# Kernel optimization log

Measured on AMD Instinct MI355X. Metric: run time of the kernel, lower is better.

## Reference

```python
import jax, jax.numpy as jnp
import numpy as np

B, T, D = 32, 512, 384
DUR_MAX = 8                 # durations drawn in [0, DUR_MAX)
MAX_OUT = T * (DUR_MAX - 1) # static upper bound on total expanded length (3584)
ALPHA = 1.0


def setup_inputs() -> dict:
    key = jax.random.key(0)
    k1, k2 = jax.random.split(key)
    x = jax.random.normal(k1, (B, T, D), dtype=jnp.float32)
    durations = jax.random.randint(k2, (B, T), 0, DUR_MAX, dtype=jnp.int32)
    return {"input": x, "durations": durations}


def reference(input, durations):
    # patched_dur = clamp(round(alpha * dur), min=0)
    patched = jnp.round(ALPHA * durations.astype(jnp.float32)).astype(jnp.int32)
    patched = jnp.maximum(patched, 0)                       # [B, T]
    cum = jnp.cumsum(patched, axis=1)                       # [B, T] exclusive-right boundaries
    total = cum[:, -1:]                                      # [B, 1] true expanded lengths

    pos = jnp.arange(MAX_OUT, dtype=jnp.int32)               # [MAX_OUT]
    # output frame j comes from token idx = first t with cum[t] > j
    idx = jax.vmap(lambda c: jnp.searchsorted(c, pos, side='right'))(cum)  # [B, MAX_OUT]
    idx = jnp.clip(idx, 0, T - 1)
    valid = pos[None, :] < total                              # [B, MAX_OUT]

    out = jnp.take_along_axis(input, idx[:, :, None], axis=1)  # [B, MAX_OUT, D]
    return jnp.where(valid[:, :, None], out, jnp.zeros((), dtype=input.dtype))
```

## Files before the change

### kernel.cpp

```cpp
#include <hip/hip_runtime.h>

typedef float v4f __attribute__((ext_vector_type(4)));

#define NB 32
#define NT 512
#define ND 384
#define MAX_OUT 3584
#define NV 96
#define TILE 64
#define BLK 256
#define PER (TILE * NV / BLK)
#define TILES_PER_B (MAX_OUT / TILE)

__global__ __launch_bounds__(NT) void lr_scan_scatter(
    const int* __restrict__ dur, int* __restrict__ totals, int* __restrict__ idxmap)
{
    __shared__ int wsum[NT / 64];
    const int b = blockIdx.x;
    const int t = threadIdx.x;
    const int lane = t & 63;
    const int w = t >> 6;

    int d = dur[b * NT + t];
    d = d > 0 ? d : 0;

    int c = d;
    #pragma unroll
    for (int off = 1; off < 64; off <<= 1) {
        int v = __shfl_up(c, off, 64);
        if (lane >= off) c += v;
    }
    if (lane == 63) wsum[w] = c;
    __syncthreads();

    int add = 0;
    for (int i = 0; i < w; ++i) add += wsum[i];
    const int cum = c + add;
    const int start = cum - d;

    int* base = idxmap + b * MAX_OUT;
    for (int j = 0; j < d; ++j) base[start + j] = t;

    if (t == NT - 1) totals[b] = cum;
}

__global__ __launch_bounds__(BLK) void lr_gather(
    const v4f* __restrict__ in, const int* __restrict__ totals,
    const int* __restrict__ idxmap, v4f* __restrict__ out)
{
    const unsigned g8 = gridDim.x >> 3;
    const unsigned blk = (blockIdx.x & 7u) * g8 + (blockIdx.x >> 3);

    const unsigned b    = blk / TILES_PER_B;
    const unsigned tile = blk - b * TILES_PER_B;
    const unsigned row0 = tile * TILE;

    __shared__ int sidx[TILE];
    __shared__ int stot;
    const int t = threadIdx.x;
    if (t < TILE) sidx[t] = idxmap[b * MAX_OUT + row0 + t];
    if (t == 0)   stot = totals[b];
    __syncthreads();

    const int nvalid = stot - (int)row0;
    const v4f* inb  = in  + (size_t)b * NT * NV;
    v4f*       outb = out + ((size_t)b * MAX_OUT + row0) * NV;

    if (nvalid >= TILE) {
        #pragma unroll
        for (int k = 0; k < PER; ++k) {
            const int i = t + k * BLK;
            const int r = i / NV;
            const int c = i - r * NV;
            const v4f v = inb[sidx[r] * NV + c];
            __builtin_nontemporal_store(v, outb + i);
        }
    } else if (nvalid <= 0) {
        const v4f z = {0.f, 0.f, 0.f, 0.f};
        #pragma unroll
        for (int k = 0; k < PER; ++k)
            __builtin_nontemporal_store(z, outb + t + k * BLK);
    } else {
        #pragma unroll
        for (int k = 0; k < PER; ++k) {
            const int i = t + k * BLK;
            const int r = i / NV;
            const int c = i - r * NV;
            v4f v = {0.f, 0.f, 0.f, 0.f};
            if (r < nvalid) v = inb[sidx[r] * NV + c];
            __builtin_nontemporal_store(v, outb + i);
        }
    }
}

extern "C" void kernel_launch(void* const* d_in, const int* in_sizes, int n_in,
                              void* d_out, int out_size, void* d_ws, size_t ws_size,
                              hipStream_t stream)
{
    const float* x   = (const float*)d_in[0];
    const int*   dur = (const int*)d_in[1];

    int* totals = (int*)d_ws;
    int* idxmap = (int*)((char*)d_ws + 128);

    lr_scan_scatter<<<NB, NT, 0, stream>>>(dur, totals, idxmap);

    const unsigned n_blk = (unsigned)NB * TILES_PER_B;
    lr_gather<<<n_blk, BLK, 0, stream>>>(
        (const v4f*)x, totals, idxmap, (v4f*)d_out);
}
```

Before: 207.7 us.

## Fuse duration scan into gather kernel with per-block binary search

```diff
diff --git a/kernel.cpp b/kernel.cpp
--- a/kernel.cpp
+++ b/kernel.cpp
@@ -12,57 +12,60 @@
 #define PER (TILE * NV / BLK)
 #define TILES_PER_B (MAX_OUT / TILE)
 
-__global__ __launch_bounds__(NT) void lr_scan_scatter(
-    const int* __restrict__ dur, int* __restrict__ totals, int* __restrict__ idxmap)
+__global__ __launch_bounds__(BLK) void lr_fused(
+    const int* __restrict__ dur, const v4f* __restrict__ in, v4f* __restrict__ out)
 {
-    __shared__ int wsum[NT / 64];
-    const int b = blockIdx.x;
-    const int t = threadIdx.x;
+    const unsigned g8  = gridDim.x >> 3;
+    const unsigned blk = (blockIdx.x & 7u) * g8 + (blockIdx.x >> 3);
+    const unsigned b    = blk / TILES_PER_B;
+    const unsigned tile = blk - b * TILES_PER_B;
+    const unsigned row0 = tile * TILE;
+
+    __shared__ int cum[NT];
+    __shared__ int wpart[BLK / 64];
+    __shared__ int sidx[TILE];
+
+    const int t    = threadIdx.x;
     const int lane = t & 63;
-    const int w = t >> 6;
+    const int w    = t >> 6;
 
-    int d = dur[b * NT + t];
-    d = d > 0 ? d : 0;
-
-    int c = d;
+    const int2 dd = ((const int2*)(dur + b * NT))[t];
+    const int d0 = dd.x > 0 ? dd.x : 0;
+    const int d1 = dd.y > 0 ? dd.y : 0;
+    const int s = d0 + d1;
+    int c = s;
     #pragma unroll
     for (int off = 1; off < 64; off <<= 1) {
         int v = __shfl_up(c, off, 64);
         if (lane >= off) c += v;
     }
-    if (lane == 63) wsum[w] = c;
+    if (lane == 63) wpart[w] = c;
+    __syncthreads();
+    int add = 0;
+    #pragma unroll
+    for (int i = 0; i < BLK / 64; ++i) if (i < w) add += wpart[i];
+    const int epfx = add + c - s;
+    cum[2 * t]     = epfx + d0;
+    cum[2 * t + 1] = epfx + d0 + d1;
     __syncthreads();
 
-    int add = 0;
-    for (int i = 0; i < w; ++i) add += wsum[i];
-    const int cum = c + add;
-    const int start = cum - d;
+    const int total = cum[NT - 1];
 
-    int* base = idxmap + b * MAX_OUT;
-    for (int j = 0; j < d; ++j) base[start + j] = t;
-
-    if (t == NT - 1) totals[b] = cum;
-}
-
-__global__ __launch_bounds__(BLK) void lr_gather(
-    const v4f* __restrict__ in, const int* __restrict__ totals,
-    const int* __restrict__ idxmap, v4f* __restrict__ out)
-{
-    const unsigned g8 = gridDim.x >> 3;
-    const unsigned blk = (blockIdx.x & 7u) * g8 + (blockIdx.x >> 3);
-
-    const unsigned b    = blk / TILES_PER_B;
-    const unsigned tile = blk - b * TILES_PER_B;
-    const unsigned row0 = tile * TILE;
-
-    __shared__ int sidx[TILE];
-    __shared__ int stot;
-    const int t = threadIdx.x;
-    if (t < TILE) sidx[t] = idxmap[b * MAX_OUT + row0 + t];
-    if (t == 0)   stot = totals[b];
+    if (t < TILE) {
+        const int pos = (int)row0 + t;
+        int lo = 0, hi = NT;
+        #pragma unroll
+        for (int step = 0; step < 10; ++step) {
+            if (lo < hi) {
+                const int mid = (lo + hi) >> 1;
+                if (cum[mid] <= pos) lo = mid + 1; else hi = mid;
+            }
+        }
+        sidx[t] = lo < NT - 1 ? lo : NT - 1;
+    }
     __syncthreads();
 
-    const int nvalid = stot - (int)row0;
+    const int nvalid = total - (int)row0;
     const v4f* inb  = in  + (size_t)b * NT * NV;
     v4f*       outb = out + ((size_t)b * MAX_OUT + row0) * NV;
 
@@ -71,8 +74,8 @@
         for (int k = 0; k < PER; ++k) {
             const int i = t + k * BLK;
             const int r = i / NV;
-            const int c = i - r * NV;
-            const v4f v = inb[sidx[r] * NV + c];
+            const int c2 = i - r * NV;
+            const v4f v = inb[sidx[r] * NV + c2];
             __builtin_nontemporal_store(v, outb + i);
         }
     } else if (nvalid <= 0) {
@@ -85,9 +88,9 @@
         for (int k = 0; k < PER; ++k) {
             const int i = t + k * BLK;
             const int r = i / NV;
-            const int c = i - r * NV;
+            const int c2 = i - r * NV;
             v4f v = {0.f, 0.f, 0.f, 0.f};
-            if (r < nvalid) v = inb[sidx[r] * NV + c];
+            if (r < nvalid) v = inb[sidx[r] * NV + c2];
             __builtin_nontemporal_store(v, outb + i);
         }
     }
@@ -97,15 +100,9 @@
                               void* d_out, int out_size, void* d_ws, size_t ws_size,
                               hipStream_t stream)
 {
-    const float* x   = (const float*)d_in[0];
-    const int*   dur = (const int*)d_in[1];
-
-    int* totals = (int*)d_ws;
-    int* idxmap = (int*)((char*)d_ws + 128);
-
-    lr_scan_scatter<<<NB, NT, 0, stream>>>(dur, totals, idxmap);
+    const int* dur = (const int*)d_in[1];
+    const v4f* x   = (const v4f*)d_in[0];
 
     const unsigned n_blk = (unsigned)NB * TILES_PER_B;
-    lr_gather<<<n_blk, BLK, 0, stream>>>(
-        (const v4f*)x, totals, idxmap, (v4f*)d_out);
+    lr_fused<<<n_blk, BLK, 0, stream>>>(dur, x, (v4f*)d_out);
 }
```

After: 206.6 us. No clear change (-0.5%).
